# Kernel optimization log

Hardware: AMD Instinct MI355X
Metric: run time of the kernel (lower is better)

The kernel has to match this reference:

```python
import jax, jax.numpy as jnp
import numpy as np
from functools import partial

V, E, H, F = 32000, 256, 512, 256  # vocab, embed_dim, hidden_dim, num_filters
FS = (3, 4, 5)

def setup_inputs() -> dict:
    key = jax.random.key(0)
    ks = jax.random.split(key, 24)
    s = 0.02
    d = {}
    d["src"] = jax.random.randint(ks[0], (32, 512), 0, V)
    d["trg"] = jax.random.randint(ks[1], (32, 64), 0, V)
    # embeddings with padding_idx=0 zeroed
    d["enc_emb"] = (jax.random.normal(ks[2], (V, E)) * s).at[0].set(0.0)
    d["dec_emb"] = (jax.random.normal(ks[3], (V, E)) * s).at[0].set(0.0)
    # conv1d weights (out_channels=F, in_channels=E, kernel)
    d["conv_w3"] = jax.random.normal(ks[4], (F, E, 3)) * s
    d["conv_b3"] = jnp.zeros((F,))
    d["conv_w4"] = jax.random.normal(ks[5], (F, E, 4)) * s
    d["conv_b4"] = jnp.zeros((F,))
    d["conv_w5"] = jax.random.normal(ks[6], (F, E, 5)) * s
    d["conv_b5"] = jnp.zeros((F,))
    d["fc1_w"] = jax.random.normal(ks[7], (H, 3 * F)) * s
    d["fc1_b"] = jnp.zeros((H,))
    d["fc2_w"] = jax.random.normal(ks[8], (H, H)) * s
    d["fc2_b"] = jnp.zeros((H,))
    # 2-layer LSTM: layer1 input E+H, layer2 input H; gates order i,f,g,o
    d["w_ih1"] = jax.random.normal(ks[9], (4 * H, E + H)) * s
    d["w_hh1"] = jax.random.normal(ks[10], (4 * H, H)) * s
    d["b_ih1"] = jnp.zeros((4 * H,))
    d["b_hh1"] = jnp.zeros((4 * H,))
    d["w_ih2"] = jax.random.normal(ks[11], (4 * H, H)) * s
    d["w_hh2"] = jax.random.normal(ks[12], (4 * H, H)) * s
    d["b_ih2"] = jnp.zeros((4 * H,))
    d["b_hh2"] = jnp.zeros((4 * H,))
    d["out_w"] = jax.random.normal(ks[13], (V, H)) * s
    d["out_b"] = jnp.zeros((V,))
    return d

def _lstm_cell(x, h, c, w_ih, w_hh, b_ih, b_hh):
    gates = x @ w_ih.T + b_ih + h @ w_hh.T + b_hh  # (B, 4H)
    i, f, g, o = jnp.split(gates, 4, axis=-1)
    c_new = jax.nn.sigmoid(f) * c + jax.nn.sigmoid(i) * jnp.tanh(g)
    h_new = jax.nn.sigmoid(o) * jnp.tanh(c_new)
    return h_new, c_new

def _encoder(src, enc_emb, convs, fc1_w, fc1_b, fc2_w, fc2_b):
    x = enc_emb[src]                    # (B, S, E)
    x = jnp.transpose(x, (0, 2, 1))     # (B, E, S)
    pooled = []
    for w, b in convs:
        y = jax.lax.conv_general_dilated(
            x, w, window_strides=(1,), padding='VALID',
            dimension_numbers=('NCH', 'OIH', 'NCH'))  # (B, F, S-k+1)
        pooled.append(jnp.max(jax.nn.relu(y + b[None, :, None]), axis=2))
    cat = jnp.concatenate(pooled, axis=1)              # (B, 3F)
    h = jax.nn.relu(cat @ fc1_w.T + fc1_b)             # (B, H)
    return h @ fc2_w.T + fc2_b                         # (B, H)

def reference(src, trg, enc_emb, conv_w3, conv_b3, conv_w4, conv_b4,
              conv_w5, conv_b5, fc1_w, fc1_b, fc2_w, fc2_b, dec_emb,
              w_ih1, w_hh1, b_ih1, b_hh1, w_ih2, w_hh2, b_ih2, b_hh2,
              out_w, out_b):
    B, T = trg.shape
    enc_out = _encoder(src, enc_emb,
                       [(conv_w3, conv_b3), (conv_w4, conv_b4), (conv_w5, conv_b5)],
                       fc1_w, fc1_b, fc2_w, fc2_b)  # (B, H)

    def step(carry, tok):
        h1, c1, h2, c2 = carry
        x = jnp.concatenate([dec_emb[tok], enc_out], axis=1)  # (B, E+H)
        h1, c1 = _lstm_cell(x, h1, c1, w_ih1, w_hh1, b_ih1, b_hh1)
        h2, c2 = _lstm_cell(h1, h2, c2, w_ih2, w_hh2, b_ih2, b_hh2)
        logits = h2 @ out_w.T + out_b                          # (B, V)
        return (h1, c1, h2, c2), logits

    z = jnp.zeros((B, H), dtype=enc_out.dtype)
    tokens = trg[:, :-1].T  # teacher forcing (ratio=1.0): (T-1, B)
    _, logits = jax.lax.scan(step, (z, z, z, z), tokens)       # (T-1, B, V)
    logits = jnp.transpose(logits, (1, 0, 2))                  # (B, T-1, V)
    # outputs[:, 0] is left as zeros, matching the torch loop starting at t=1
    return jnp.concatenate([jnp.zeros((B, 1, logits.shape[-1]), logits.dtype), logits], axis=1)
```

## Files before the change

### kernel.cpp

```cpp
#include <hip/hip_runtime.h>
#include <math.h>
#include <stdint.h>

#define B_    32
#define E_    256
#define F_    256
#define H_    512
#define V_    32000
#define G4    2048

typedef unsigned short u16;
typedef unsigned long long u64;
typedef __attribute__((ext_vector_type(8))) short bf16x8;
typedef __attribute__((ext_vector_type(4))) float f32x4;

__device__ __forceinline__ float fsig(float x) {
  return __builtin_amdgcn_rcpf(1.f + __expf(-x));
}
__device__ __forceinline__ float ftanh(float x) {
  return 1.f - 2.f * __builtin_amdgcn_rcpf(1.f + __expf(2.f * x));
}

__device__ __forceinline__ u16 f2bf(float f) {
  uint32_t u = __float_as_uint(f);
  uint32_t r = (u + 0x7FFFu + ((u >> 16) & 1u)) >> 16;
  return (u16)r;
}
__device__ __forceinline__ uint32_t pack2(float a, float b) {
  return (uint32_t)f2bf(a) | ((uint32_t)f2bf(b) << 16);
}

#define GLOAD16(gp, lp) __builtin_amdgcn_global_load_lds( \
    (const __attribute__((address_space(1))) uint32_t*)(const void*)(gp), \
    (__attribute__((address_space(3))) uint32_t*)(void*)(lp), 16, 0, 0)

#define ALOAD(P) __hip_atomic_load((P), __ATOMIC_RELAXED, __HIP_MEMORY_SCOPE_AGENT)
#define ASTORE(P, V) __hip_atomic_store((P), (V), __ATOMIC_RELAXED, __HIP_MEMORY_SCOPE_AGENT)

__global__ void init_all(float* pooled, uint32_t* sent1, uint32_t* sent2,
                         u16* h1d, u16* h2a,
                         const float* bi1, const float* bh1,
                         const float* bi2, const float* bh2,
                         float* bs1, float* bs2, float* out) {
  int i = blockIdx.x * blockDim.x + threadIdx.x, st = gridDim.x * blockDim.x;
  for (int k = i; k < 24576; k += st) pooled[k] = 0.f;
  for (int k = i; k < 131072; k += st) {
    uint32_t v = (k < 2048 && (k & 15) == 0) ? 1u : 0u;
    sent1[k] = v; sent2[k] = v;
  }
  uint4 z = {0u, 0u, 0u, 0u};
  for (int k = i; k < 2048; k += st) { ((uint4*)h1d)[k] = z; ((uint4*)h2a)[k] = z; }
  for (int k = i; k < G4; k += st) { bs1[k] = bi1[k] + bh1[k]; bs2[k] = bi2[k] + bh2[k]; }
  for (int k = i; k < B_ * V_; k += st) {
    int b = k / V_, v = k - b * V_;
    out[(size_t)b * 64 * V_ + v] = 0.f;
  }
}

__global__ void cvt_all(const float* s0, u16* d0, const float* s1, u16* d1,
                        const float* s2, u16* d2, const float* s3, u16* d3,
                        const float* s4, u16* d4) {
  int i = blockIdx.x * blockDim.x + threadIdx.x, st = gridDim.x * blockDim.x;
  for (; i < 2637824; i += st) {
    int j = i; const float* s; u16* d;
    if (j < 2048000) { s = s0; d = d0; }
    else if ((j -= 2048000) < 196608) { s = s1; d = d1; }
    else if ((j -= 196608) < 131072) { s = s2; d = d2; }
    else if ((j -= 131072) < 131072) { s = s3; d = d3; }
    else { j -= 131072; s = s4; d = d4; }
    const float4* sp = (const float4*)s + 2 * (size_t)j;
    float4 a = sp[0], b = sp[1];
    uint4 u;
    u.x = pack2(a.x, a.y); u.y = pack2(a.z, a.w);
    u.z = pack2(b.x, b.y); u.w = pack2(b.z, b.w);
    *((uint4*)d + j) = u;
  }
}

__global__ void wtj_all(const float* w3, u16* t3, const float* w4, u16* t4,
                        const float* w5, u16* t5) {
  int i = blockIdx.x * blockDim.x + threadIdx.x, st = gridDim.x * blockDim.x;
  for (; i < 786432; i += st) {
    int j = i; const float* w; u16* wt; int kw;
    if (j < 196608) { w = w3; wt = t3; kw = 3; }
    else if ((j -= 196608) < 262144) { w = w4; wt = t4; kw = 4; }
    else { j -= 262144; w = w5; wt = t5; kw = 5; }
    int f = j / (kw * 256);
    int r = j - f * (kw * 256);
    int jj = r >> 8, e = r & 255;
    wt[j] = f2bf(w[(f * 256 + e) * kw + jj]);
  }
}

__global__ void build_x1(const int* __restrict__ trg, const float* __restrict__ demb,
                         const float* __restrict__ enco, u16* __restrict__ X1) {
  int r = blockIdx.x, tid = threadIdx.x;
  u16* row = X1 + (size_t)r * 768;
  if (r >= 2016) { row[tid] = 0; row[256 + tid] = 0; row[512 + tid] = 0; return; }
  int t = r >> 5, b = r & 31;
  int tok = trg[b * 64 + t];
  row[tid]       = f2bf(demb[(size_t)tok * E_ + tid]);
  row[256 + tid] = f2bf(enco[b * H_ + tid]);
  row[512 + tid] = f2bf(enco[b * H_ + 256 + tid]);
}

__global__ void gemm_small(const float* __restrict__ A, const float* __restrict__ W,
                           const float* __restrict__ bias, float* __restrict__ C,
                           int K, int N, int relu) {
  int nl = threadIdx.x & 7, b = threadIdx.x >> 3;
  int n = blockIdx.x * 8 + nl;
  const float* a = A + b * K;
  const float* w = W + (size_t)n * K;
  float acc = 0.f;
  for (int k = 0; k < K; k += 4) {
    float4 av = *reinterpret_cast<const float4*>(&a[k]);
    float4 wv = *reinterpret_cast<const float4*>(&w[k]);
    acc = fmaf(av.x, wv.x, acc); acc = fmaf(av.y, wv.y, acc);
    acc = fmaf(av.z, wv.z, acc); acc = fmaf(av.w, wv.w, acc);
  }
  acc += bias[n];
  if (relu) acc = fmaxf(acc, 0.f);
  C[b * N + n] = acc;
}

template<int RM>
__global__ __launch_bounds__(256)
void gemm_mfma(const u16* __restrict__ A, const u16* __restrict__ Bw,
               const float* __restrict__ bias, float* __restrict__ C,
               int M, int N, int K) {
  __shared__ char smem[32768];
  const int tid = threadIdx.x;
  const int wid = tid >> 6, lane = tid & 63;
  const int hi = lane >> 4, lo = lane & 15;
  const int wr = wid >> 1, wc = wid & 1;
  const int m0 = blockIdx.x * 128, n0 = blockIdx.y * 128;
  const int NT = K >> 5;
  const int srow = lane >> 2, sc = lane & 3;

  f32x4 acc[4][4];
#pragma unroll
  for (int i = 0; i < 4; ++i)
#pragma unroll
    for (int j = 0; j < 4; ++j) acc[i][j] = (f32x4){0.f, 0.f, 0.f, 0.f};

  for (int t = -1; t < NT; ++t) {
    int ts = t + 1;
    if (ts < NT) {
      char* base = smem + (ts & 1) * 16384;
      int k0 = ts << 5;
#pragma unroll
      for (int q = 0; q < 2; ++q) {
        int row = (wid + q * 4) * 16 + srow;
        int gc = sc ^ (row & 3);
        const char* gp = (const char*)A + (((size_t)(m0 + row) * K + k0) << 1) + gc * 16;
        GLOAD16(gp, base + (wid + q * 4) * 1024);
      }
#pragma unroll
      for (int q = 0; q < 2; ++q) {
        int row = (wid + q * 4) * 16 + srow;
        int gc = sc ^ (row & 3);
        const char* gp = (const char*)Bw + (((size_t)(n0 + row) * K + k0) << 1) + gc * 16;
        GLOAD16(gp, base + 8192 + (wid + q * 4) * 1024);
      }
    }
    if (t >= 0) {
      char* base = smem + (t & 1) * 16384;
      bf16x8 af[4], bfr[4];
#pragma unroll
      for (int mi = 0; mi < 4; ++mi) {
        int row = wr * 64 + mi * 16 + lo;
        af[mi] = *(const bf16x8*)(base + row * 64 + ((hi ^ (row & 3)) << 4));
      }
#pragma unroll
      for (int ni = 0; ni < 4; ++ni) {
        int row = wc * 64 + ni * 16 + lo;
        bfr[ni] = *(const bf16x8*)(base + 8192 + row * 64 + ((hi ^ (row & 3)) << 4));
      }
#pragma unroll
      for (int mi = 0; mi < 4; ++mi)
#pragma unroll
        for (int ni = 0; ni < 4; ++ni)
          acc[mi][ni] = __builtin_amdgcn_mfma_f32_16x16x32_bf16(af[mi], bfr[ni], acc[mi][ni], 0, 0, 0);
    }
    __syncthreads();
  }

#pragma unroll
  for (int mi = 0; mi < 4; ++mi)
#pragma unroll
    for (int r = 0; r < 4; ++r) {
      int m = m0 + wr * 64 + mi * 16 + hi * 4 + r;
      if (m >= M) continue;
      size_t rowbase;
      if (RM == 1) { int t2 = m >> 5, b = m & 31; rowbase = ((size_t)b * 64 + t2 + 1) * (size_t)V_; }
      else rowbase = (size_t)m * N;
#pragma unroll
      for (int ni = 0; ni < 4; ++ni) {
        int col = n0 + wc * 64 + ni * 16 + lo;
        C[rowbase + col] = acc[mi][r == 0 ? ni : ni][r] + bias[col];
      }
    }
}

__global__ __launch_bounds__(256)
void conv_mfma(const u16* __restrict__ wt3, const u16* __restrict__ wt4,
               const u16* __restrict__ wt5,
               const float* __restrict__ cb3, const float* __restrict__ cb4,
               const float* __restrict__ cb5,
               float* __restrict__ pooled,
               const int* __restrict__ srcTok, const float* __restrict__ emb) {
  const int z = blockIdx.z;
  const u16* Bw = (z == 0) ? wt3 : (z == 1) ? wt4 : wt5;
  const float* bias = (z == 0) ? cb3 : (z == 1) ? cb4 : cb5;
  const int K = 768 + 256 * z, kw = 3 + z, poolOff = 256 * z;

  __shared__ char smem[32768];
  const int tid = threadIdx.x;
  const int wid = tid >> 6, lane = tid & 63;
  const int hi = lane >> 4, lo = lane & 15;
  const int wr = wid >> 1, wc = wid & 1;
  const int m0 = blockIdx.x * 128, n0 = blockIdx.y * 128;
  const int NT = K >> 5;
  const int srow = lane >> 2, sc = lane & 3;

  f32x4 acc[4][4];
#pragma unroll
  for (int i = 0; i < 4; ++i)
#pragma unroll
    for (int j = 0; j < 4; ++j) acc[i][j] = (f32x4){0.f, 0.f, 0.f, 0.f};

  for (int t = -1; t < NT; ++t) {
    int ts = t + 1;
    if (ts < NT) {
      char* base = smem + (ts & 1) * 16384;
      int k0 = ts << 5;
      {
        int j = k0 >> 8, e0 = k0 & 255;
        int row = tid >> 1;
        int m = m0 + row;
        int s = m & 511, b = m >> 9;
        int sj = s + j;
        int tok = (sj < 512) ? srcTok[b * 512 + sj] : -1;
#pragma unroll
        for (int q = 0; q < 2; ++q) {
          int cg = (tid & 1) * 2 + q;
          uint4 u;
          if (tok >= 0) {
            const float* ep = emb + (size_t)tok * 256 + e0 + cg * 8;
            float4 f0 = *(const float4*)(ep);
            float4 f1 = *(const float4*)(ep + 4);
            u.x = pack2(f0.x, f0.y); u.y = pack2(f0.z, f0.w);
            u.z = pack2(f1.x, f1.y); u.w = pack2(f1.z, f1.w);
          } else u = (uint4){0, 0, 0, 0};
          int c = cg ^ (row & 3);
          *(uint4*)(base + row * 64 + c * 16) = u;
        }
      }
#pragma unroll
      for (int q = 0; q < 2; ++q) {
        int row = (wid + q * 4) * 16 + srow;
        int gc = sc ^ (row & 3);
        const char* gp = (const char*)Bw + (((size_t)(n0 + row) * K + k0) << 1) + gc * 16;
        GLOAD16(gp, base + 8192 + (wid + q * 4) * 1024);
      }
    }
    if (t >= 0) {
      char* base = smem + (t & 1) * 16384;
      bf16x8 af[4], bfr[4];
#pragma unroll
      for (int mi = 0; mi < 4; ++mi) {
        int row = wr * 64 + mi * 16 + lo;
        af[mi] = *(const bf16x8*)(base + row * 64 + ((hi ^ (row & 3)) << 4));
      }
#pragma unroll
      for (int ni = 0; ni < 4; ++ni) {
        int row = wc * 64 + ni * 16 + lo;
        bfr[ni] = *(const bf16x8*)(base + 8192 + row * 64 + ((hi ^ (row & 3)) << 4));
      }
#pragma unroll
      for (int mi = 0; mi < 4; ++mi)
#pragma unroll
        for (int ni = 0; ni < 4; ++ni)
          acc[mi][ni] = __builtin_amdgcn_mfma_f32_16x16x32_bf16(af[mi], bfr[ni], acc[mi][ni], 0, 0, 0);
    }
    __syncthreads();
  }

  int b = m0 >> 9;
  int slim = 512 - kw;
#pragma unroll
  for (int ni = 0; ni < 4; ++ni) {
    int col = n0 + wc * 64 + ni * 16 + lo;
    float bv = bias[col];
    float mx = 0.f;
#pragma unroll
    for (int mi = 0; mi < 4; ++mi)
#pragma unroll
      for (int r = 0; r < 4; ++r) {
        int m = m0 + wr * 64 + mi * 16 + hi * 4 + r;
        int s = m & 511;
        float v = acc[mi][ni][r] + bv;
        if (s <= slim && v > mx) mx = v;
      }
    atomicMax((int*)&pooled[b * 768 + poolOff + col], __float_as_int(mx));
  }
}

__global__ __launch_bounds__(256, 1)
void lstm_fused(const float* __restrict__ pre,
                const u16* __restrict__ whh1,
                const u16* __restrict__ wih2, const u16* __restrict__ whh2,
                const float* __restrict__ bs2,
                uint32_t* __restrict__ sent1, uint32_t* __restrict__ sent2,
                u16* __restrict__ h1d, u16* __restrict__ h2a) {
  __shared__ char smem[74752];
  const int tid = threadIdx.x;
  const int wid = tid >> 6, lane = tid & 63, hi = lane >> 4, lo = lane & 15;
  const int hrow = tid >> 3, k8 = tid & 7;
  const int pb = hrow, pj0 = k8 * 2;

#define WAVE_DRAIN() asm volatile("s_waitcnt vmcnt(0)" ::: "memory")
#define POLL1(P) while (ALOAD(P) == 0u) __builtin_amdgcn_s_sleep(1);
#define POLL2(P, Q) for (;;) { uint32_t x_ = ALOAD(P), y_ = ALOAD(Q); \
                               if (x_ & y_) break; __builtin_amdgcn_s_sleep(1); }

  if (blockIdx.x < 32) {
    const int bi = blockIdx.x;
    u16* hlds = (u16*)smem;
    float* glds = (float*)(smem + 33280);

    bf16x8 wreg[16];
    const u16* wp = whh1 + (((size_t)(wid * 512 + bi * 16 + lo)) << 9) + hi * 8;
#pragma unroll
    for (int ks = 0; ks < 16; ++ks) wreg[ks] = *(const bf16x8*)(wp + ks * 32);

    float creg0 = 0.f, creg1 = 0.f;

    for (int t = 0; t < 63; ++t) {
      const float* pr = pre + (((size_t)(t * 32 + pb)) << 11) + bi * 16 + pj0;
      float pi0 = pr[0], pf0 = pr[512], pg0 = pr[1024], po0 = pr[1536];
      float pi1 = pr[1], pf1 = pr[513], pg1 = pr[1025], po1 = pr[1537];

      const u64* hp = (const u64*)(h1d + ((size_t)t * 32 + hrow) * 512);
      f32x4 acc0 = (f32x4){0.f,0.f,0.f,0.f}, acc1 = (f32x4){0.f,0.f,0.f,0.f};

      POLL1(sent1 + (size_t)t * 2048 + lane * 16)
      {
        u64 v[8];
#pragma unroll
        for (int g = 0; g < 4; ++g) {
          int c = k8 + 8 * g;
          v[2*g]   = ALOAD(hp + 2 * c);
          v[2*g+1] = ALOAD(hp + 2 * c + 1);
        }
#pragma unroll
        for (int g = 0; g < 4; ++g) {
          int c = k8 + 8 * g;
          u64 w2[2] = { v[2*g], v[2*g+1] };
          *(uint4*)(hlds + hrow * 520 + c * 8) = *(const uint4*)w2;
        }
      }
      __syncthreads();
#pragma unroll
      for (int ks = 0; ks < 8; ++ks) {
        int cg = (ks * 4 + hi) * 8;
        bf16x8 a0 = *(const bf16x8*)(hlds + lo * 520 + cg);
        bf16x8 a1 = *(const bf16x8*)(hlds + (16 + lo) * 520 + cg);
        acc0 = __builtin_amdgcn_mfma_f32_16x16x32_bf16(a0, wreg[ks], acc0, 0, 0, 0);
        acc1 = __builtin_amdgcn_mfma_f32_16x16x32_bf16(a1, wreg[ks], acc1, 0, 0, 0);
      }
      POLL1(sent1 + (size_t)t * 2048 + (64 + lane) * 16)
      {
        u64 v[8];
#pragma unroll
        for (int g = 0; g < 4; ++g) {
          int c = 32 + k8 + 8 * g;
          v[2*g]   = ALOAD(hp + 2 * c);
          v[2*g+1] = ALOAD(hp + 2 * c + 1);
        }
#pragma unroll
        for (int g = 0; g < 4; ++g) {
          int c = 32 + k8 + 8 * g;
          u64 w2[2] = { v[2*g], v[2*g+1] };
          *(uint4*)(hlds + hrow * 520 + c * 8) = *(const uint4*)w2;
        }
      }
      __syncthreads();
#pragma unroll
      for (int ks = 8; ks < 16; ++ks) {
        int cg = (ks * 4 + hi) * 8;
        bf16x8 a0 = *(const bf16x8*)(hlds + lo * 520 + cg);
        bf16x8 a1 = *(const bf16x8*)(hlds + (16 + lo) * 520 + cg);
        acc0 = __builtin_amdgcn_mfma_f32_16x16x32_bf16(a0, wreg[ks], acc0, 0, 0, 0);
        acc1 = __builtin_amdgcn_mfma_f32_16x16x32_bf16(a1, wreg[ks], acc1, 0, 0, 0);
      }
#pragma unroll
      for (int r = 0; r < 4; ++r) {
        glds[wid * 544 + (hi * 4 + r) * 17 + lo] = acc0[r];
        glds[wid * 544 + (16 + hi * 4 + r) * 17 + lo] = acc1[r];
      }
      __syncthreads();

      float iv0 = glds[0*544 + pb*17 + pj0]   + pi0, fv0 = glds[1*544 + pb*17 + pj0]   + pf0;
      float gv0 = glds[2*544 + pb*17 + pj0]   + pg0, ov0 = glds[3*544 + pb*17 + pj0]   + po0;
      float iv1 = glds[0*544 + pb*17 + pj0+1] + pi1, fv1 = glds[1*544 + pb*17 + pj0+1] + pf1;
      float gv1 = glds[2*544 + pb*17 + pj0+1] + pg1, ov1 = glds[3*544 + pb*17 + pj0+1] + po1;
      float cn0 = fsig(fv0) * creg0 + fsig(iv0) * ftanh(gv0);
      float hn0 = fsig(ov0) * ftanh(cn0);
      float cn1 = fsig(fv1) * creg1 + fsig(iv1) * ftanh(gv1);
      float hn1 = fsig(ov1) * ftanh(cn1);
      creg0 = cn0; creg1 = cn1;
      ASTORE((uint32_t*)(h1d + ((size_t)(t + 1) * 32 + pb) * 512 + bi * 16 + pj0),
             pack2(hn0, hn1));
      WAVE_DRAIN();
      if (lane == 0)
        ASTORE(sent1 + (size_t)(t + 1) * 2048 + (bi * 4 + wid) * 16, 1u);
    }
  } else {
    const int bi2 = blockIdx.x - 32;
    u16* alds = (u16*)smem;
    float* glds = (float*)(smem + 66048);

    bf16x8 wreg[32];
    {
      const u16* wa = wih2 + (((size_t)(wid * 512 + bi2 * 16 + lo)) << 9) + hi * 8;
      const u16* wb = whh2 + (((size_t)(wid * 512 + bi2 * 16 + lo)) << 9) + hi * 8;
#pragma unroll
      for (int ks = 0; ks < 16; ++ks) {
        wreg[ks]      = *(const bf16x8*)(wa + ks * 32);
        wreg[16 + ks] = *(const bf16x8*)(wb + ks * 32);
      }
    }
    float bsv0 = bs2[0 * 512 + bi2 * 16 + pj0], bsv0b = bs2[0 * 512 + bi2 * 16 + pj0 + 1];
    float bsv1 = bs2[1 * 512 + bi2 * 16 + pj0], bsv1b = bs2[1 * 512 + bi2 * 16 + pj0 + 1];
    float bsv2 = bs2[2 * 512 + bi2 * 16 + pj0], bsv2b = bs2[2 * 512 + bi2 * 16 + pj0 + 1];
    float bsv3 = bs2[3 * 512 + bi2 * 16 + pj0], bsv3b = bs2[3 * 512 + bi2 * 16 + pj0 + 1];

    float creg0 = 0.f, creg1 = 0.f;

    for (int t = 0; t < 63; ++t) {
      f32x4 acc0 = (f32x4){0.f,0.f,0.f,0.f}, acc1 = (f32x4){0.f,0.f,0.f,0.f};

      POLL2(sent1 + (size_t)(t + 1) * 2048 + lane * 16,
            sent1 + (size_t)(t + 1) * 2048 + (64 + lane) * 16)
      {
        const u64* hp1 = (const u64*)(h1d + ((size_t)(t + 1) * 32 + hrow) * 512);
        u64 v[16];
#pragma unroll
        for (int g = 0; g < 8; ++g) {
          int c = k8 + 8 * g;
          v[2*g]   = ALOAD(hp1 + 2 * c);
          v[2*g+1] = ALOAD(hp1 + 2 * c + 1);
        }
#pragma unroll
        for (int g = 0; g < 8; ++g) {
          int c = k8 + 8 * g;
          u64 w2[2] = { v[2*g], v[2*g+1] };
          *(uint4*)(alds + hrow * 1032 + c * 8) = *(const uint4*)w2;
        }
      }
      __syncthreads();
#pragma unroll
      for (int ks = 0; ks < 16; ++ks) {
        int cg = (ks * 4 + hi) * 8;
        bf16x8 a0 = *(const bf16x8*)(alds + lo * 1032 + cg);
        bf16x8 a1 = *(const bf16x8*)(alds + (16 + lo) * 1032 + cg);
        acc0 = __builtin_amdgcn_mfma_f32_16x16x32_bf16(a0, wreg[ks], acc0, 0, 0, 0);
        acc1 = __builtin_amdgcn_mfma_f32_16x16x32_bf16(a1, wreg[ks], acc1, 0, 0, 0);
      }
      POLL2(sent2 + (size_t)t * 2048 + lane * 16,
            sent2 + (size_t)t * 2048 + (64 + lane) * 16)
      {
        const u64* hp2 = (const u64*)(h2a + ((size_t)t * 32 + hrow) * 512);
        u64 v[16];
#pragma unroll
        for (int g = 0; g < 8; ++g) {
          int c = k8 + 8 * g;
          v[2*g]   = ALOAD(hp2 + 2 * c);
          v[2*g+1] = ALOAD(hp2 + 2 * c + 1);
        }
#pragma unroll
        for (int g = 0; g < 8; ++g) {
          int c = 64 + k8 + 8 * g;
          u64 w2[2] = { v[2*g], v[2*g+1] };
          *(uint4*)(alds + hrow * 1032 + c * 8) = *(const uint4*)w2;
        }
      }
      __syncthreads();
#pragma unroll
      for (int ks = 0; ks < 16; ++ks) {
        int cg = (64 + ks * 4 + hi) * 8;
        bf16x8 a0 = *(const bf16x8*)(alds + lo * 1032 + cg);
        bf16x8 a1 = *(const bf16x8*)(alds + (16 + lo) * 1032 + cg);
        acc0 = __builtin_amdgcn_mfma_f32_16x16x32_bf16(a0, wreg[16 + ks], acc0, 0, 0, 0);
        acc1 = __builtin_amdgcn_mfma_f32_16x16x32_bf16(a1, wreg[16 + ks], acc1, 0, 0, 0);
      }
#pragma unroll
      for (int r = 0; r < 4; ++r) {
        glds[wid * 544 + (hi * 4 + r) * 17 + lo] = acc0[r];
        glds[wid * 544 + (16 + hi * 4 + r) * 17 + lo] = acc1[r];
      }
      __syncthreads();

      float gi0 = glds[0*544 + pb*17 + pj0]   + bsv0,  gf0 = glds[1*544 + pb*17 + pj0]   + bsv1;
      float gg0 = glds[2*544 + pb*17 + pj0]   + bsv2,  go0 = glds[3*544 + pb*17 + pj0]   + bsv3;
      float gi1 = glds[0*544 + pb*17 + pj0+1] + bsv0b, gf1 = glds[1*544 + pb*17 + pj0+1] + bsv1b;
      float gg1 = glds[2*544 + pb*17 + pj0+1] + bsv2b, go1 = glds[3*544 + pb*17 + pj0+1] + bsv3b;
      float cn0 = fsig(gf0) * creg0 + fsig(gi0) * ftanh(gg0);
      float hn0 = fsig(go0) * ftanh(cn0);
      float cn1 = fsig(gf1) * creg1 + fsig(gi1) * ftanh(gg1);
      float hn1 = fsig(go1) * ftanh(cn1);
      creg0 = cn0; creg1 = cn1;
      ASTORE((uint32_t*)(h2a + ((size_t)(t + 1) * 32 + pb) * 512 + bi2 * 16 + pj0),
             pack2(hn0, hn1));
      WAVE_DRAIN();
      if (lane == 0)
        ASTORE(sent2 + (size_t)(t + 1) * 2048 + (bi2 * 4 + wid) * 16, 1u);
    }
  }
#undef POLL1
#undef POLL2
#undef WAVE_DRAIN
}

extern "C" void kernel_launch(void* const* d_in, const int* in_sizes, int n_in,
                              void* d_out, int out_size, void* d_ws, size_t ws_size,
                              hipStream_t stream) {
  const int*   src  = (const int*)  d_in[0];
  const int*   trg  = (const int*)  d_in[1];
  const float* eemb = (const float*)d_in[2];
  const float* demb = (const float*)d_in[3];
  const float* cw3  = (const float*)d_in[4];
  const float* cb3  = (const float*)d_in[5];
  const float* cw4  = (const float*)d_in[6];
  const float* cb4  = (const float*)d_in[7];
  const float* cw5  = (const float*)d_in[8];
  const float* cb5  = (const float*)d_in[9];
  const float* fc1w = (const float*)d_in[10];
  const float* fc1b = (const float*)d_in[11];
  const float* fc2w = (const float*)d_in[12];
  const float* fc2b = (const float*)d_in[13];
  const float* wih1 = (const float*)d_in[14];
  const float* whh1 = (const float*)d_in[15];
  const float* bih1 = (const float*)d_in[16];
  const float* bhh1 = (const float*)d_in[17];
  const float* wih2 = (const float*)d_in[18];
  const float* whh2 = (const float*)d_in[19];
  const float* bih2 = (const float*)d_in[20];
  const float* bhh2 = (const float*)d_in[21];
  const float* outw = (const float*)d_in[22];
  const float* outb = (const float*)d_in[23];
  float* out = (float*)d_out;

  uint32_t* sent1 = (uint32_t*)d_ws;
  uint32_t* sent2 = sent1 + 131072;
  u16* h1d      = (u16*)(sent2 + 131072);
  u16* h2a      = h1d + 1048576;
  float* pooled = (float*)(h2a + 1048576);
  float* ench   = pooled + 24576;
  float* enco   = ench + 16384;
  float* bs1    = enco + 16384;
  float* bs2    = bs1 + 2048;
  float* pre    = bs2 + 2048;
  u16* outw_bf  = (u16*)(pre + 4128768);
  u16* wih1_bf  = outw_bf + 16384000;
  u16* wih2_bf  = wih1_bf + 1572864;
  u16* whh1_bf  = wih2_bf + 1048576;
  u16* whh2_bf  = whh1_bf + 1048576;
  u16* wtj3     = whh2_bf + 1048576;
  u16* wtj4     = wtj3 + 196608;
  u16* wtj5     = wtj4 + 262144;
  u16* X1       = wtj5 + 327680;

  init_all<<<512, 256, 0, stream>>>(pooled, sent1, sent2, h1d, h2a,
                                    bih1, bhh1, bih2, bhh2, bs1, bs2, out);
  cvt_all<<<2048, 256, 0, stream>>>(outw, outw_bf, wih1, wih1_bf, wih2, wih2_bf,
                                    whh1, whh1_bf, whh2, whh2_bf);
  wtj_all<<<512, 256, 0, stream>>>(cw3, wtj3, cw4, wtj4, cw5, wtj5);

  conv_mfma<<<dim3(128, 2, 3), 256, 0, stream>>>(wtj3, wtj4, wtj5, cb3, cb4, cb5,
                                                 pooled, src, eemb);
  gemm_small<<<64, 256, 0, stream>>>(pooled, fc1w, fc1b, ench, 768, 512, 1);
  gemm_small<<<64, 256, 0, stream>>>(ench, fc2w, fc2b, enco, 512, 512, 0);

  build_x1<<<2048, 256, 0, stream>>>(trg, demb, enco, X1);
  gemm_mfma<0><<<dim3(16, 16), 256, 0, stream>>>(X1, wih1_bf, bs1, pre, 2016, 2048, 768);
  lstm_fused<<<64, 256, 0, stream>>>(pre, whh1_bf, wih2_bf, whh2_bf, bs2,
                                     sent1, sent2, h1d, h2a);
  gemm_mfma<1><<<dim3(16, 250), 256, 0, stream>>>(h2a + 16384, outw_bf, outb, out,
                                                  2016, V_, 512);
}
```

Before: 545.2 us.

## Fuse output projection GEMM into LSTM kernel and overlap it with recurrence

Adds 160 extra blocks to the persistent LSTM kernel. They poll the layer-2 sentinel flags and compute output-vocab GEMM tiles as soon as the hidden states for each 4-timestep row tile are ready, instead of launching a separate GEMM after the recurrence. This is meant to hide the large output projection behind the serial LSTM time loop. The risk is that the extra blocks compete for CUs and memory bandwidth with the latency-bound recurrence blocks. Progress also depends on all 224 blocks being co-resident, and the polling could slow the critical path.

```diff
diff --git a/kernel.cpp b/kernel.cpp
--- a/kernel.cpp
+++ b/kernel.cpp
@@ -123,7 +123,6 @@
   C[b * N + n] = acc;
 }
 
-template<int RM>
 __global__ __launch_bounds__(256)
 void gemm_mfma(const u16* __restrict__ A, const u16* __restrict__ Bw,
                const float* __restrict__ bias, float* __restrict__ C,
@@ -191,13 +190,11 @@
     for (int r = 0; r < 4; ++r) {
       int m = m0 + wr * 64 + mi * 16 + hi * 4 + r;
       if (m >= M) continue;
-      size_t rowbase;
-      if (RM == 1) { int t2 = m >> 5, b = m & 31; rowbase = ((size_t)b * 64 + t2 + 1) * (size_t)V_; }
-      else rowbase = (size_t)m * N;
+      size_t rowbase = (size_t)m * N;
 #pragma unroll
       for (int ni = 0; ni < 4; ++ni) {
         int col = n0 + wc * 64 + ni * 16 + lo;
-        C[rowbase + col] = acc[mi][r == 0 ? ni : ni][r] + bias[col];
+        C[rowbase + col] = acc[mi][ni][r] + bias[col];
       }
     }
 }
@@ -312,7 +309,9 @@
                 const u16* __restrict__ wih2, const u16* __restrict__ whh2,
                 const float* __restrict__ bs2,
                 uint32_t* __restrict__ sent1, uint32_t* __restrict__ sent2,
-                u16* __restrict__ h1d, u16* __restrict__ h2a) {
+                u16* __restrict__ h1d, u16* __restrict__ h2a,
+                const u16* __restrict__ outw_bf, const float* __restrict__ outb,
+                float* __restrict__ out) {
   __shared__ char smem[74752];
   const int tid = threadIdx.x;
   const int wid = tid >> 6, lane = tid & 63, hi = lane >> 4, lo = lane & 15;
@@ -323,6 +322,8 @@
 #define POLL1(P) while (ALOAD(P) == 0u) __builtin_amdgcn_s_sleep(1);
 #define POLL2(P, Q) for (;;) { uint32_t x_ = ALOAD(P), y_ = ALOAD(Q); \
                                if (x_ & y_) break; __builtin_amdgcn_s_sleep(1); }
+#define POLL2S(P, Q) for (;;) { uint32_t x_ = ALOAD(P), y_ = ALOAD(Q); \
+                                if (x_ & y_) break; __builtin_amdgcn_s_sleep(16); }
 
   if (blockIdx.x < 32) {
     const int bi = blockIdx.x;
@@ -416,7 +417,7 @@
       if (lane == 0)
         ASTORE(sent1 + (size_t)(t + 1) * 2048 + (bi * 4 + wid) * 16, 1u);
     }
-  } else {
+  } else if (blockIdx.x < 64) {
     const int bi2 = blockIdx.x - 32;
     u16* alds = (u16*)smem;
     float* glds = (float*)(smem + 66048);
@@ -517,9 +518,88 @@
       if (lane == 0)
         ASTORE(sent2 + (size_t)(t + 1) * 2048 + (bi2 * 4 + wid) * 16, 1u);
     }
+  } else {
+    const int bid2 = blockIdx.x - 64;
+    const int wr = wid >> 1, wc = wid & 1;
+    const int srow = lane >> 2, sc = lane & 3;
+    const u16* A = h2a + 16384;
+
+    for (int w = bid2; w < 16 * 250; w += 160) {
+      int rt = w / 250, ct = w - rt * 250;
+      int tf = rt * 4 + 4; if (tf > 63) tf = 63;
+      if (wid == 0)
+        POLL2S(sent2 + (size_t)tf * 2048 + lane * 16,
+               sent2 + (size_t)tf * 2048 + (64 + lane) * 16)
+      __syncthreads();
+
+      const int m0 = rt * 128, n0 = ct * 128;
+      f32x4 acc[4][4];
+#pragma unroll
+      for (int i = 0; i < 4; ++i)
+#pragma unroll
+        for (int j = 0; j < 4; ++j) acc[i][j] = (f32x4){0.f, 0.f, 0.f, 0.f};
+
+      for (int t = -1; t < 16; ++t) {
+        int ts = t + 1;
+        if (ts < 16) {
+          char* base = smem + (ts & 1) * 16384;
+          int k0 = ts << 5;
+#pragma unroll
+          for (int q = 0; q < 2; ++q) {
+            int row = (wid + q * 4) * 16 + srow;
+            int gc = sc ^ (row & 3);
+            const char* gp = (const char*)A + (((size_t)(m0 + row) * 512 + k0) << 1) + gc * 16;
+            GLOAD16(gp, base + (wid + q * 4) * 1024);
+          }
+#pragma unroll
+          for (int q = 0; q < 2; ++q) {
+            int row = (wid + q * 4) * 16 + srow;
+            int gc = sc ^ (row & 3);
+            const char* gp = (const char*)outw_bf + (((size_t)(n0 + row) * 512 + k0) << 1) + gc * 16;
+            GLOAD16(gp, base + 8192 + (wid + q * 4) * 1024);
+          }
+        }
+        if (t >= 0) {
+          char* base = smem + (t & 1) * 16384;
+          bf16x8 af[4], bfr[4];
+#pragma unroll
+          for (int mi = 0; mi < 4; ++mi) {
+            int row = wr * 64 + mi * 16 + lo;
+            af[mi] = *(const bf16x8*)(base + row * 64 + ((hi ^ (row & 3)) << 4));
+          }
+#pragma unroll
+          for (int ni = 0; ni < 4; ++ni) {
+            int row = wc * 64 + ni * 16 + lo;
+            bfr[ni] = *(const bf16x8*)(base + 8192 + row * 64 + ((hi ^ (row & 3)) << 4));
+          }
+#pragma unroll
+          for (int mi = 0; mi < 4; ++mi)
+#pragma unroll
+            for (int ni = 0; ni < 4; ++ni)
+              acc[mi][ni] = __builtin_amdgcn_mfma_f32_16x16x32_bf16(af[mi], bfr[ni], acc[mi][ni], 0, 0, 0);
+        }
+        __syncthreads();
+      }
+
+#pragma unroll
+      for (int mi = 0; mi < 4; ++mi)
+#pragma unroll
+        for (int r = 0; r < 4; ++r) {
+          int m = m0 + wr * 64 + mi * 16 + hi * 4 + r;
+          if (m >= 2016) continue;
+          int t2 = m >> 5, b = m & 31;
+          size_t rowbase = ((size_t)b * 64 + t2 + 1) * (size_t)V_;
+#pragma unroll
+          for (int ni = 0; ni < 4; ++ni) {
+            int col = n0 + wc * 64 + ni * 16 + lo;
+            out[rowbase + col] = acc[mi][ni][r] + outb[col];
+          }
+        }
+    }
   }
 #undef POLL1
 #undef POLL2
+#undef POLL2S
 #undef WAVE_DRAIN
 }
 
@@ -584,9 +664,7 @@
   gemm_small<<<64, 256, 0, stream>>>(ench, fc2w, fc2b, enco, 512, 512, 0);
 
   build_x1<<<2048, 256, 0, stream>>>(trg, demb, enco, X1);
-  gemm_mfma<0><<<dim3(16, 16), 256, 0, stream>>>(X1, wih1_bf, bs1, pre, 2016, 2048, 768);
-  lstm_fused<<<64, 256, 0, stream>>>(pre, whh1_bf, wih2_bf, whh2_bf, bs2,
-                                     sent1, sent2, h1d, h2a);
-  gemm_mfma<1><<<dim3(16, 250), 256, 0, stream>>>(h2a + 16384, outw_bf, outb, out,
-                                                  2016, V_, 512);
-}
+  gemm_mfma<<<dim3(16, 16), 256, 0, stream>>>(X1, wih1_bf, bs1, pre, 2016, 2048, 768);
+  lstm_fused<<<224, 256, 0, stream>>>(pre, whh1_bf, wih2_bf, whh2_bf, bs2,
+                                      sent1, sent2, h1d, h2a, outw_bf, outb, out);
+}
```

Result: faster. 471.3 us (-13.6%).
